# Optimization experiments

Hardware: AMD Instinct MI355X
Metric: run time of the kernel (lower is better)

The kernel has to match this reference:

```python
import jax, jax.numpy as jnp
import numpy as np

B, H, S, D = 1, 16, 2048, 64
KQ_PRE, KK_PRE = 6, 11      # pre-softmax conv kernel (query x key)
KQ_POST, KK_POST = 3, 3     # post-softmax conv kernel


def depthwise_causal_conv(x, w):
    """Per-head 2D conv over score tensor x:[B,H,Q,K], w:[H,kq,kk].
    Causal padding: only past queries (pad top kq-1) and past keys (pad left kk-1)."""
    h, kq, kk = w.shape
    return jax.lax.conv_general_dilated(
        x, w[:, None, :, :],  # [H,1,kq,kk] depthwise
        window_strides=(1, 1),
        padding=[(kq - 1, 0), (kk - 1, 0)],
        dimension_numbers=("NCHW", "OIHW", "NCHW"),
        feature_group_count=h,
    )


def setup_inputs() -> dict:
    key = jax.random.key(0)
    ks = jax.random.split(key, 8)
    eye = jnp.eye(H, dtype=jnp.float32)
    return {
        "xq": jax.random.normal(ks[0], (B, H, S, D), jnp.float32),
        "xk": jax.random.normal(ks[1], (B, H, S, D), jnp.float32),
        "xv": jax.random.normal(ks[2], (B, H, S, D), jnp.float32),
        "mask": jnp.zeros((1,), jnp.float32),  # unused (use_mask=False)
        "w_conv_pre": 0.1 * jax.random.normal(ks[3], (H, KQ_PRE, KK_PRE), jnp.float32),
        "w_conv_post": 0.1 * jax.random.normal(ks[4], (H, KQ_POST, KK_POST), jnp.float32),
        "w_psm": eye + 0.02 * jax.random.normal(ks[5], (H, H), jnp.float32),
        "w_posm": eye + 0.02 * jax.random.normal(ks[6], (H, H), jnp.float32),
    }


def reference(xq, xk, xv, mask, w_conv_pre, w_conv_post, w_psm, w_posm):
    del mask  # use_mask=False path
    b, h, q, d = xq.shape
    k = xk.shape[2]
    causal = jnp.arange(k)[None, :] <= jnp.arange(q)[:, None]  # [Q,K] True = visible
    scale = 1.0 / jnp.sqrt(jnp.float32(d))

    # QK^T scores
    scores = jnp.einsum("bhqd,bhkd->bhqk", xq, xk) * scale
    # pre-softmax causal depthwise conv (future entries zeroed going in)
    scores = depthwise_causal_conv(jnp.where(causal, scores, 0.0), w_conv_pre)
    # pre-softmax per-head linear mixing; masked region -> -inf (output_value)
    scores = jnp.einsum("gh,bhqk->bgqk", w_psm, scores)
    scores = jnp.where(causal, scores, -jnp.inf)

    probs = jax.nn.softmax(scores.astype(jnp.float32), axis=-1).astype(xq.dtype)

    # post-softmax causal depthwise conv
    probs = depthwise_causal_conv(jnp.where(causal, probs, 0.0), w_conv_post)
    probs = jnp.where(causal, probs, 0.0)
    # post-softmax per-head linear mixing; masked region -> 0
    probs = jnp.einsum("gh,bhqk->bgqk", w_posm, probs)
    probs = jnp.where(causal, probs, 0.0)

    # attention output, transposed to [B,S,H,D]
    out = jnp.einsum("bhqk,bhkd->bqhd", probs, xv)
    return out
```

## Files before the change

### kernel.cpp

```cpp
#include <hip/hip_runtime.h>
#include <math.h>

#define H 16
#define S 2048
#define D 64
#define SCALEQK 0.125f
#define CH 256

typedef __attribute__((ext_vector_type(4))) float f32x4;
typedef __attribute__((ext_vector_type(8))) short bf16x8;
typedef __attribute__((ext_vector_type(8))) _Float16 f16x8;
typedef __attribute__((ext_vector_type(4))) _Float16 f16x4;
typedef __attribute__((ext_vector_type(2))) _Float16 f16x2;

__device__ inline float h2f(unsigned short b) {
    _Float16 h; __builtin_memcpy(&h, &b, 2); return (float)h;
}
__device__ inline unsigned short f2h(float x) {
    _Float16 h = (_Float16)x; unsigned short b; __builtin_memcpy(&b, &h, 2); return b;
}
__device__ inline unsigned int pack2h(float a, float b) {
    return (unsigned int)f2h(a) | ((unsigned int)f2h(b) << 16);
}

__device__ inline float fdot2f(unsigned int a, unsigned int b, float c) {
#if __has_builtin(__builtin_amdgcn_fdot2)
    f16x2 av, bv;
    __builtin_memcpy(&av, &a, 4);
    __builtin_memcpy(&bv, &b, 4);
    return __builtin_amdgcn_fdot2(av, bv, c, false);
#else
    return c + h2f((unsigned short)(a & 0xffff)) * h2f((unsigned short)(b & 0xffff))
             + h2f((unsigned short)(a >> 16))    * h2f((unsigned short)(b >> 16));
#endif
}

__device__ inline void stage_hilo(float4 a, float4 b, uint4* vh, uint4* vl) {
    float xs[8] = {a.x, a.y, a.z, a.w, b.x, b.y, b.z, b.w};
    unsigned int hh[8], ll[8];
#pragma unroll
    for (int j = 0; j < 8; ++j) {
        unsigned int u = __float_as_uint(xs[j]);
        unsigned int h = (u + 0x7fffu + ((u >> 16) & 1u)) >> 16;
        float r = xs[j] - __uint_as_float(h << 16);
        unsigned int u2 = __float_as_uint(r);
        hh[j] = h;
        ll[j] = (u2 + 0x7fffu + ((u2 >> 16) & 1u)) >> 16;
    }
    uint4 h4, l4;
    h4.x = hh[0] | (hh[1] << 16); h4.y = hh[2] | (hh[3] << 16);
    h4.z = hh[4] | (hh[5] << 16); h4.w = hh[6] | (hh[7] << 16);
    l4.x = ll[0] | (ll[1] << 16); l4.y = ll[2] | (ll[3] << 16);
    l4.z = ll[4] | (ll[5] << 16); l4.w = ll[6] | (ll[7] << 16);
    *vh = h4; *vl = l4;
}

__device__ inline void online_upd(float& m, float& l, float x) {
    if (x > m) { l = l * __expf(m - x) + 1.f; m = x; }
    else       { l += __expf(x - m); }
}

__global__ __launch_bounds__(256) void mta_cvt_kernel(const float* __restrict__ src,
                                                      unsigned short* __restrict__ hi,
                                                      unsigned short* __restrict__ lo,
                                                      float scale, int n8) {
    int i = blockIdx.x * 256 + threadIdx.x;
    int stride = gridDim.x * 256;
    for (; i < n8; i += stride) {
        const float* p = src + (size_t)i * 8;
        float4 a = *(const float4*)p;
        float4 b = *(const float4*)(p + 4);
        a.x *= scale; a.y *= scale; a.z *= scale; a.w *= scale;
        b.x *= scale; b.y *= scale; b.z *= scale; b.w *= scale;
        uint4 vh, vl; stage_hilo(a, b, &vh, &vl);
        *(uint4*)&hi[(size_t)i * 8] = vh;
        *(uint4*)&lo[(size_t)i * 8] = vl;
    }
}

__global__ __launch_bounds__(256) void mta_vt_kernel(const float* __restrict__ xv,
                                                     unsigned short* __restrict__ vt) {
    const int kt = blockIdx.x, f = blockIdx.y;
    const int tid = threadIdx.x;
    __shared__ unsigned short lt[64][65];
#pragma unroll
    for (int i = 0; i < 16; ++i) {
        int idx = tid + i * 256;
        int r = idx >> 6, c = idx & 63;
        lt[r][c] = f2h(xv[((size_t)f * S + kt * 64 + r) * D + c]);
    }
    __syncthreads();
#pragma unroll
    for (int i = 0; i < 16; ++i) {
        int idx = tid + i * 256;
        int d = idx >> 6, k = idx & 63;
        vt[((size_t)f * D + d) * S + kt * 64 + k] = lt[k][d];
    }
}

__global__ __launch_bounds__(256) void mta_gemm_kernel(
        const unsigned short* __restrict__ qhi, const unsigned short* __restrict__ qlo,
        const unsigned short* __restrict__ khi, const unsigned short* __restrict__ klo,
        unsigned short* __restrict__ R, int qs, int SQ) {
    const int kt = blockIdx.x, qt = blockIdx.y, h = blockIdx.z;
    const int q0 = qs - 64 + qt * 64;
    const int k0 = kt * 64;
    if (k0 > q0 + 68) return;
    const int tid = threadIdx.x;
    const int SQ64 = SQ + 64;

    __shared__ unsigned short Qs[2][64][72];
    __shared__ unsigned short Ks[2][64][72];
    __shared__ unsigned short Ro[64][72];

    {
        int r = tid >> 2, d = (tid & 3) * 16;
        int gq = q0 + r;
        uint4 z = {0u, 0u, 0u, 0u};
        uint4 a0 = z, a1 = z, b0 = z, b1 = z;
        if (gq >= 0) {
            size_t off = ((size_t)h * S + gq) * D + d;
            a0 = *(const uint4*)&qhi[off]; a1 = *(const uint4*)&qhi[off + 8];
            b0 = *(const uint4*)&qlo[off]; b1 = *(const uint4*)&qlo[off + 8];
        }
        *(uint4*)&Qs[0][r][d] = a0; *(uint4*)&Qs[0][r][d + 8] = a1;
        *(uint4*)&Qs[1][r][d] = b0; *(uint4*)&Qs[1][r][d + 8] = b1;
        size_t offk = ((size_t)h * S + (k0 + r)) * D + d;
        uint4 c0 = *(const uint4*)&khi[offk];
        uint4 c1 = *(const uint4*)&khi[offk + 8];
        uint4 d0 = *(const uint4*)&klo[offk];
        uint4 d1 = *(const uint4*)&klo[offk + 8];
        *(uint4*)&Ks[0][r][d] = c0; *(uint4*)&Ks[0][r][d + 8] = c1;
        *(uint4*)&Ks[1][r][d] = d0; *(uint4*)&Ks[1][r][d + 8] = d1;
    }
    __syncthreads();

    const int w = tid >> 6, lane = tid & 63;
    const int wr = w >> 1, wc = w & 1;
    const int lr = lane & 15, lk = lane >> 4;

    f32x4 acc[2][2];
#pragma unroll
    for (int mi = 0; mi < 2; ++mi)
#pragma unroll
        for (int ni = 0; ni < 2; ++ni) acc[mi][ni] = (f32x4){0.f, 0.f, 0.f, 0.f};

#pragma unroll
    for (int ks = 0; ks < 2; ++ks) {
        int db = ks * 32 + lk * 8;
#pragma unroll
        for (int mi = 0; mi < 2; ++mi) {
            bf16x8 ah = *(const bf16x8*)&Qs[0][wr * 32 + mi * 16 + lr][db];
            bf16x8 al = *(const bf16x8*)&Qs[1][wr * 32 + mi * 16 + lr][db];
#pragma unroll
            for (int ni = 0; ni < 2; ++ni) {
                bf16x8 bh = *(const bf16x8*)&Ks[0][wc * 32 + ni * 16 + lr][db];
                bf16x8 bl = *(const bf16x8*)&Ks[1][wc * 32 + ni * 16 + lr][db];
                acc[mi][ni] = __builtin_amdgcn_mfma_f32_16x16x32_bf16(ah, bh, acc[mi][ni], 0, 0, 0);
                acc[mi][ni] = __builtin_amdgcn_mfma_f32_16x16x32_bf16(ah, bl, acc[mi][ni], 0, 0, 0);
                acc[mi][ni] = __builtin_amdgcn_mfma_f32_16x16x32_bf16(al, bh, acc[mi][ni], 0, 0, 0);
            }
        }
    }

#pragma unroll
    for (int mi = 0; mi < 2; ++mi)
#pragma unroll
        for (int ni = 0; ni < 2; ++ni)
#pragma unroll
            for (int i = 0; i < 4; ++i) {
                int row = wr * 32 + mi * 16 + lk * 4 + i;
                int col = wc * 32 + ni * 16 + lr;
                int gq = q0 + row, gk = k0 + col;
                Ro[row][col] = f2h((gk <= gq) ? acc[mi][ni][i] : 0.f);
            }
    __syncthreads();

#pragma unroll
    for (int ii = 0; ii < 2; ++ii) {
        int idx = tid + ii * 256;
        int row = idx >> 3, c8 = (idx & 7) * 8;
        int lrow = qt * 64 + row;
        *(uint4*)&R[((size_t)h * SQ64 + lrow) * S + k0 + c8] = *(const uint4*)&Ro[row][c8];
    }
}

__global__ __launch_bounds__(256) void mta_convmix_kernel(
        const unsigned short* __restrict__ R,
        const float* __restrict__ w_pre, const float* __restrict__ w_psm,
        unsigned short* __restrict__ sc, int qs, int SQ) {
    const int kc = blockIdx.x, qt = blockIdx.y;
    const int q0 = qs - 16 + qt * 16;
    const int k0 = kc * 64;
    if (k0 > q0 + 15) return;
    const int tid = threadIdx.x;
    const int SQ64 = SQ + 64;

    __shared__ unsigned short raw_u16[2][2][21][88];
    __shared__ unsigned short co[1024][16];
    __shared__ unsigned int wpk[16][6][6];
    __shared__ unsigned short wpsmf[16][16];

    for (int idx = tid; idx < 576; idx += 256) {
        int h = idx / 36, i2 = (idx % 36) / 6, ip = idx % 6;
        float w0 = w_pre[h * 66 + i2 * 11 + ip * 2];
        float w1 = (ip < 5) ? w_pre[h * 66 + i2 * 11 + ip * 2 + 1] : 0.f;
        wpk[h][i2][ip] = pack2h(w0, w1);
    }
    wpsmf[tid >> 4][tid & 15] = f2h(w_psm[tid]);

    const int ql = tid & 15;
    const int kb = (tid >> 4) * 4;

    const int sr = tid / 10, sc8 = tid % 10;
    const bool sact = (tid < 210);
    const bool sval = sact && (k0 + sc8 * 8 >= 16);
    const size_t srow_off = (size_t)(qt * 16 + sr + 43) * S + (k0 - 16 + sc8 * 8);

    uint4 sA = {0u, 0u, 0u, 0u}, sB = {0u, 0u, 0u, 0u};

#define LOADC(hh, dst) do { \
        if (sval) dst = *(const uint4*)&R[(size_t)(hh) * SQ64 * S + srow_off]; \
        else { dst.x = 0u; dst.y = 0u; dst.z = 0u; dst.w = 0u; } \
    } while (0)

#define WRITEC(bb, tt, src) do { if (sact) { \
        *(uint4*)&raw_u16[bb][tt][sr][sc8 * 8] = src; } \
    } while (0)

#define CONVC(hh, bb, tt) do { \
        float c0_ = 0.f, c1_ = 0.f, c2_ = 0.f, c3_ = 0.f; \
        _Pragma("unroll") \
        for (int i2_ = 0; i2_ < 6; ++i2_) { \
            const unsigned int* rp_ = \
                (const unsigned int*)&raw_u16[bb][tt][ql + i2_][0] + (kb / 2 + 3); \
            unsigned int P_[7]; \
            _Pragma("unroll") \
            for (int i_ = 0; i_ < 7; ++i_) P_[i_] = rp_[i_]; \
            unsigned int Sv_[6]; \
            _Pragma("unroll") \
            for (int i_ = 0; i_ < 6; ++i_) Sv_[i_] = (P_[i_] >> 16) | (P_[i_ + 1] << 16); \
            unsigned int T_ = P_[6] >> 16; \
            const unsigned int* wp_ = &wpk[hh][i2_][0]; \
            _Pragma("unroll") \
            for (int i_ = 0; i_ < 6; ++i_) { \
                unsigned int w_ = wp_[i_]; \
                c0_ = fdot2f(w_, P_[i_], c0_); \
                c1_ = fdot2f(w_, Sv_[i_], c1_); \
                c2_ = fdot2f(w_, P_[i_ + 1], c2_); \
                c3_ = fdot2f(w_, (i_ < 5) ? Sv_[i_ + 1] : T_, c3_); \
            } \
        } \
        { float cc_[4] = {c0_, c1_, c2_, c3_}; \
          int p0_ = ql * 64 + kb; \
          _Pragma("unroll") \
          for (int j_ = 0; j_ < 4; ++j_) { \
              int pp_ = p0_ + j_; \
              int x_ = ((pp_ >> 2) ^ (pp_ >> 6)) & 3; \
              co[pp_][(hh) ^ (x_ << 2)] = f2h(cc_[j_]); } } \
    } while (0)

    LOADC(0, sA);
    LOADC(1, sB);
    WRITEC(0, 0, sA);
    WRITEC(0, 1, sB);
    __syncthreads();
    for (int ph = 0; ph < 8; ++ph) {
        int bb = ph & 1;
        if (ph < 7) { LOADC(2 * ph + 2, sA); LOADC(2 * ph + 3, sB); }
        CONVC(2 * ph,     bb, 0);
        CONVC(2 * ph + 1, bb, 1);
        if (ph < 7) { WRITEC(bb ^ 1, 0, sA); WRITEC(bb ^ 1, 1, sB); }
        __syncthreads();
    }
#undef LOADC
#undef WRITEC
#undef CONVC

    const int lane = tid & 63, wv = tid >> 6;
    const int hg = lane >> 4;
#if __has_builtin(__builtin_amdgcn_mfma_f32_16x16x16f16)
    f16x4 afrag = *(const f16x4*)&wpsmf[lane & 15][hg * 4];
    for (int t = wv; t < 64; t += 4) {
        int p = t * 16 + (lane & 15);
        int x = ((p >> 2) ^ (p >> 6)) & 3;
        f16x4 bfrag = *(const f16x4*)&co[p][(hg ^ x) << 2];
        f32x4 d = {0.f, 0.f, 0.f, 0.f};
        d = __builtin_amdgcn_mfma_f32_16x16x16f16(afrag, bfrag, d, 0, 0, 0);
        int qq = q0 + (p >> 6);
        int kk = k0 + (p & 63);
        int srow = qt * 16 + (p >> 6);
#pragma unroll
        for (int i = 0; i < 4; ++i) {
            int g = hg * 4 + i;
            sc[((size_t)(g * (SQ + 16) + srow)) * S + kk] =
                f2h((kk <= qq) ? d[i] : 0.f);
        }
    }
#else
    for (int t = wv; t < 64; t += 4) {
        int p = t * 16 + (lane & 15);
        int x = ((p >> 2) ^ (p >> 6)) & 3;
        float ch[16];
#pragma unroll
        for (int a = 0; a < 4; ++a) {
            f16x4 b4 = *(const f16x4*)&co[p][(a ^ x) << 2];
#pragma unroll
            for (int tt = 0; tt < 4; ++tt) ch[a * 4 + tt] = (float)b4[tt];
        }
        int qq = q0 + (p >> 6);
        int kk = k0 + (p & 63);
        int srow = qt * 16 + (p >> 6);
#pragma unroll
        for (int i = 0; i < 4; ++i) {
            int g = hg * 4 + i;
            float s = 0.f;
#pragma unroll
            for (int hh = 0; hh < 16; ++hh) s += h2f(wpsmf[g][hh]) * ch[hh];
            sc[((size_t)(g * (SQ + 16) + srow)) * S + kk] =
                f2h((kk <= qq) ? s : 0.f);
        }
    }
#endif
}

__global__ __launch_bounds__(256) void mta_rowstats_kernel(
        const unsigned short* __restrict__ sc,
        float* __restrict__ mrow, float* __restrict__ rlrow, int qs, int SQ) {
    int row = blockIdx.x * 4 + (threadIdx.x >> 6);
    int lane = threadIdx.x & 63;
    int g = row / SQ, qq = row % SQ;
    int q = qs + qq;
    const unsigned short* rp = sc + ((size_t)(g * (SQ + 16) + qq + 16)) * S;

    float v[32];
#pragma unroll
    for (int it = 0; it < 4; ++it) {
        int kbase = it * 512 + lane * 8;
        if (it * 512 <= q) {
            uint4 u = *(const uint4*)&rp[kbase];
            unsigned int ws[4] = {u.x, u.y, u.z, u.w};
#pragma unroll
            for (int j = 0; j < 4; ++j) {
                float x0 = h2f((unsigned short)(ws[j] & 0xffff));
                float x1 = h2f((unsigned short)(ws[j] >> 16));
                v[it * 8 + 2 * j]     = (kbase + 2 * j     <= q) ? x0 : -INFINITY;
                v[it * 8 + 2 * j + 1] = (kbase + 2 * j + 1 <= q) ? x1 : -INFINITY;
            }
        } else {
#pragma unroll
            for (int j = 0; j < 8; ++j) v[it * 8 + j] = -INFINITY;
        }
    }
    float m = -INFINITY;
#pragma unroll
    for (int j = 0; j < 32; ++j) m = fmaxf(m, v[j]);
#pragma unroll
    for (int off = 1; off < 64; off <<= 1) m = fmaxf(m, __shfl_xor(m, off));
    float l = 0.f;
#pragma unroll
    for (int j = 0; j < 32; ++j) l += __expf(v[j] - m);
#pragma unroll
    for (int off = 1; off < 64; off <<= 1) l += __shfl_xor(l, off);
    if (lane == 0) { mrow[g * S + q] = m; rlrow[g * S + q] = 1.f / l; }
}

__global__ __launch_bounds__(256) void mta_out2_kernel(
        const unsigned short* __restrict__ sc,
        const float* __restrict__ mrow, const float* __restrict__ rlrow,
        const unsigned short* __restrict__ vt,
        const float* __restrict__ w_post, const float* __restrict__ w_posm,
        float* __restrict__ out, int qs, int SQ) {
    const int qt = blockIdx.x, kc = blockIdx.y;
    const int q0 = qs + qt * 16;
    const int kstart = kc * CH;
    if (kstart > q0 + 15) return;
    const int kend = min(kstart + CH, q0 + 16);
    const int tid = threadIdx.x;

    __shared__ unsigned short ps[16][18][36];
    __shared__ unsigned short pm2[16][16][40];
    __shared__ float mst[16][18], rst[16][18];
    __shared__ float wpost_s[144], wposm_s[256];

    wposm_s[tid] = w_posm[tid];
    if (tid < 144) wpost_s[tid] = w_post[tid];
    for (int i = tid; i < 288; i += 256) {
        int g = i / 18, r = i % 18;
        int qp = q0 - 2 + r;
        if (qp >= 0) { mst[g][r] = mrow[g * S + qp]; rst[g][r] = rlrow[g * S + qp]; }
        else         { mst[g][r] = 0.f; rst[g][r] = 0.f; }
    }

    const int ql = tid >> 4, kb = (tid & 15) * 2;
    const int wv = tid >> 6, lane = tid & 63;
    const int lr = lane & 15, lk = lane >> 4;

    f32x4 acc[4][4];
#pragma unroll
    for (int a = 0; a < 4; ++a)
#pragma unroll
        for (int b = 0; b < 4; ++b) acc[a][b] = (f32x4){0.f, 0.f, 0.f, 0.f};

    __syncthreads();

    for (int k0 = kstart; k0 < kend; k0 += 32) {
        for (int i = tid; i < 4896; i += 256) {
            int g = i / 306, rem = i % 306;
            int r = rem / 17, c2 = (rem % 17) * 2;
            int qp = q0 - 2 + r;
            int kp = k0 - 2 + c2;
            float p0 = 0.f, p1 = 0.f;
            if (qp >= 0 && kp >= 0) {
                unsigned int u = *(const unsigned int*)
                    &sc[((size_t)(g * (SQ + 16) + qp - (qs - 16))) * S + kp];
                float mm = mst[g][r], rr = rst[g][r];
                if (kp <= qp)     p0 = __expf(h2f((unsigned short)(u & 0xffff)) - mm) * rr;
                if (kp + 1 <= qp) p1 = __expf(h2f((unsigned short)(u >> 16)) - mm) * rr;
            }
            *(unsigned int*)&ps[g][r][c2] = pack2h(p0, p1);
        }
        __syncthreads();

        {
            float cg0[16], cg1[16];
#pragma unroll
            for (int g = 0; g < 16; ++g) {
                float c0 = 0.f, c1 = 0.f;
#pragma unroll
                for (int i2 = 0; i2 < 3; ++i2) {
                    unsigned int u0 = *(const unsigned int*)&ps[g][ql + i2][kb];
                    unsigned int u1 = *(const unsigned int*)&ps[g][ql + i2][kb + 2];
                    float v0 = h2f((unsigned short)(u0 & 0xffff));
                    float v1 = h2f((unsigned short)(u0 >> 16));
                    float v2 = h2f((unsigned short)(u1 & 0xffff));
                    float v3 = h2f((unsigned short)(u1 >> 16));
                    const float* wp = &wpost_s[g * 9 + i2 * 3];
                    c0 += wp[0] * v0 + wp[1] * v1 + wp[2] * v2;
                    c1 += wp[0] * v1 + wp[1] * v2 + wp[2] * v3;
                }
                cg0[g] = c0; cg1[g] = c1;
            }
            int q = q0 + ql, k = k0 + kb;
            bool val0 = (k <= q) && (k < kend);
            bool val1 = (k + 1 <= q) && (k + 1 < kend);
#pragma unroll
            for (int ff = 0; ff < 16; ++ff) {
                float s0 = 0.f, s1 = 0.f;
#pragma unroll
                for (int g = 0; g < 16; ++g) {
                    float w = wposm_s[ff * 16 + g];
                    s0 += w * cg0[g]; s1 += w * cg1[g];
                }
                *(unsigned int*)&pm2[ff][ql][kb] = pack2h(val0 ? s0 : 0.f, val1 ? s1 : 0.f);
            }
        }
        __syncthreads();

#pragma unroll
        for (int hh = 0; hh < 4; ++hh) {
            int f = wv * 4 + hh;
            f16x8 a = *(const f16x8*)&pm2[f][lr][lk * 8];
#pragma unroll
            for (int tc = 0; tc < 4; ++tc) {
                uint4 braw = *(const uint4*)
                    &vt[((size_t)(f * D + tc * 16 + lr)) * S + k0 + lk * 8];
                f16x8 b;
                __builtin_memcpy(&b, &braw, 16);
                acc[hh][tc] = __builtin_amdgcn_mfma_f32_16x16x32_f16(a, b, acc[hh][tc], 0, 0, 0);
            }
        }
    }

#pragma unroll
    for (int hh = 0; hh < 4; ++hh) {
        int f = wv * 4 + hh;
#pragma unroll
        for (int tc = 0; tc < 4; ++tc) {
#pragma unroll
            for (int i = 0; i < 4; ++i) {
                int q = q0 + lk * 4 + i;
                int d = tc * 16 + lr;
                atomicAdd(&out[((size_t)q * H + f) * D + d], acc[hh][tc][i]);
            }
        }
    }
}

__global__ __launch_bounds__(256) void fb_stats_kernel(
        const float* __restrict__ xq, const float* __restrict__ xk,
        const float* __restrict__ w_pre, const float* __restrict__ w_psm,
        float* __restrict__ mpart, float* __restrict__ lpart) {
    const int kc = blockIdx.x, qt = blockIdx.y;
    const int q0 = qt * 16;
    const int kstart = kc * CH;
    if (kstart > q0 + 15) return;
    const int kend = min(kstart + CH, q0 + 16);
    const int tid = threadIdx.x;

    __shared__ unsigned short Qs[2][32][72];
    __shared__ unsigned short Ks[2][48][72];
    __shared__ float raws[32][50];
    __shared__ float wpre_s[16 * 66];
    __shared__ float wpsm_s[256];

    for (int i = tid; i < 16 * 66; i += 256) wpre_s[i] = w_pre[i];
    wpsm_s[tid] = w_psm[tid];

    const int ql = tid >> 4;
    const int kb = (tid & 15) * 2;
    const int q = q0 + ql;

    float mreg[16], lreg[16];
#pragma unroll
    for (int g = 0; g < 16; ++g) { mreg[g] = -INFINITY; lreg[g] = 0.f; }

    for (int k0 = kstart; k0 < kend; k0 += 32) {
        float acc0[16], acc1[16];
#pragma unroll
        for (int g = 0; g < 16; ++g) { acc0[g] = 0.f; acc1[g] = 0.f; }

        for (int h = 0; h < H; ++h) {
            {
                int r = tid >> 3, d = (tid & 7) * 8;
                int qp = q0 - 5 + r;
                float4 a = {0,0,0,0}, b = {0,0,0,0};
                if (r < 21 && qp >= 0) {
                    const float* p = &xq[(h * S + qp) * D + d];
                    a = *(const float4*)p; b = *(const float4*)(p + 4);
                }
                uint4 vh, vl; stage_hilo(a, b, &vh, &vl);
                *(uint4*)&Qs[0][r][d] = vh;
                *(uint4*)&Qs[1][r][d] = vl;
            }
            for (int i = tid; i < 384; i += 256) {
                int r = i >> 3, d = (i & 7) * 8;
                int kp = k0 - 10 + r;
                float4 a = {0,0,0,0}, b = {0,0,0,0};
                if (r < 42 && kp >= 0) {
                    const float* p = &xk[(h * S + kp) * D + d];
                    a = *(const float4*)p; b = *(const float4*)(p + 4);
                }
                uint4 vh, vl; stage_hilo(a, b, &vh, &vl);
                *(uint4*)&Ks[0][r][d] = vh;
                *(uint4*)&Ks[1][r][d] = vl;
            }
            __syncthreads();
            {
                int w = tid >> 6, l = tid & 63;
                int lr = l & 15, lk = l >> 4;
                for (int t = w; t < 6; t += 4) {
                    int tr = t / 3, tc = t % 3;
                    f32x4 acc = {0.f, 0.f, 0.f, 0.f};
#pragma unroll
                    for (int ks = 0; ks < 2; ++ks) {
                        int db = ks * 32 + lk * 8;
                        bf16x8 ah = *(const bf16x8*)&Qs[0][tr * 16 + lr][db];
                        bf16x8 al = *(const bf16x8*)&Qs[1][tr * 16 + lr][db];
                        bf16x8 bh = *(const bf16x8*)&Ks[0][tc * 16 + lr][db];
                        bf16x8 bl = *(const bf16x8*)&Ks[1][tc * 16 + lr][db];
                        acc = __builtin_amdgcn_mfma_f32_16x16x32_bf16(ah, bh, acc, 0, 0, 0);
                        acc = __builtin_amdgcn_mfma_f32_16x16x32_bf16(ah, bl, acc, 0, 0, 0);
                        acc = __builtin_amdgcn_mfma_f32_16x16x32_bf16(al, bh, acc, 0, 0, 0);
                    }
#pragma unroll
                    for (int i = 0; i < 4; ++i) {
                        int row = tr * 16 + lk * 4 + i;
                        int col = tc * 16 + lr;
                        int qp = q0 - 5 + row, kp = k0 - 10 + col;
                        raws[row][col] = (kp >= 0 && kp <= qp) ? acc[i] * SCALEQK : 0.f;
                    }
                }
            }
            __syncthreads();
            {
                float c0 = 0.f, c1 = 0.f;
#pragma unroll
                for (int i2 = 0; i2 < 6; ++i2) {
                    const float* rp = &raws[ql + i2][kb];
                    float v[12];
#pragma unroll
                    for (int j = 0; j < 6; ++j) {
                        float2 t = *(const float2*)(rp + 2 * j);
                        v[2 * j] = t.x; v[2 * j + 1] = t.y;
                    }
                    const float* wp = &wpre_s[h * 66 + i2 * 11];
#pragma unroll
                    for (int j = 0; j < 11; ++j) { c0 += wp[j] * v[j]; c1 += wp[j] * v[j + 1]; }
                }
#pragma unroll
                for (int g = 0; g < 16; ++g) {
                    float wg = wpsm_s[g * 16 + h];
                    acc0[g] += wg * c0; acc1[g] += wg * c1;
                }
            }
        }
        int kk = k0 + kb;
#pragma unroll
        for (int g = 0; g < 16; ++g) {
            if (kk <= q)     online_upd(mreg[g], lreg[g], acc0[g]);
            if (kk + 1 <= q) online_upd(mreg[g], lreg[g], acc1[g]);
        }
    }
#pragma unroll
    for (int g = 0; g < 16; ++g) {
        float m = mreg[g], l = lreg[g];
#pragma unroll
        for (int off = 1; off < 16; off <<= 1) {
            float m2 = __shfl_xor(m, off);
            float l2 = __shfl_xor(l, off);
            float nm = fmaxf(m, m2);
            float t1 = (l  > 0.f) ? l  * __expf(m  - nm) : 0.f;
            float t2 = (l2 > 0.f) ? l2 * __expf(m2 - nm) : 0.f;
            m = nm; l = t1 + t2;
        }
        if ((tid & 15) == 0) {
            mpart[((size_t)kc * H + g) * S + q] = m;
            lpart[((size_t)kc * H + g) * S + q] = l;
        }
    }
}

__global__ __launch_bounds__(256) void fb_reduce_kernel(
        const float* __restrict__ mpart, const float* __restrict__ lpart,
        float* __restrict__ mrow, float* __restrict__ rlrow) {
    int r = blockIdx.x * 256 + threadIdx.x;
    if (r >= H * S) return;
    int q = r & (S - 1);
    int nkc = (q >> 8) + 1;
    float m = -INFINITY;
    for (int kc = 0; kc < nkc; ++kc) m = fmaxf(m, mpart[(size_t)kc * H * S + r]);
    float l = 0.f;
    for (int kc = 0; kc < nkc; ++kc) {
        float li = lpart[(size_t)kc * H * S + r];
        float mi = mpart[(size_t)kc * H * S + r];
        if (li > 0.f) l += li * __expf(mi - m);
    }
    mrow[r] = m;
    rlrow[r] = 1.f / l;
}

__global__ __launch_bounds__(256) void fb_out_kernel(
        const float* __restrict__ xq, const float* __restrict__ xk,
        const float* __restrict__ xv,
        const float* __restrict__ w_pre, const float* __restrict__ w_psm,
        const float* __restrict__ w_post, const float* __restrict__ w_posm,
        const float* __restrict__ mrow, const float* __restrict__ rlrow,
        float* __restrict__ out) {
    const int qt = blockIdx.x, kc = blockIdx.y;
    const int q0 = qt * 8;
    const int kstart = kc * CH;
    if (kstart > q0 + 7) return;
    const int kend = min(kstart + CH, q0 + 8);
    const int tid = threadIdx.x;

    __shared__ unsigned short Qs[2][16][72];
    __shared__ unsigned short Ks[2][48][72];
    __shared__ float raws[16][50];
    __shared__ float ps[8][10][35];
    __shared__ float m2s[16][8][33];
    __shared__ float mst[16][10], rst[16][10];
    __shared__ float wpre_s[16 * 66], wpsm_s[256], wpost_s[144], wposm_s[256];

    for (int i = tid; i < 16 * 66; i += 256) wpre_s[i] = w_pre[i];
    wpsm_s[tid] = w_psm[tid];
    wposm_s[tid] = w_posm[tid];
    if (tid < 144) wpost_s[tid] = w_post[tid];
    for (int i = tid; i < 160; i += 256) {
        int g = i / 10, r = i % 10;
        int qp = q0 - 2 + r;
        if (qp >= 0) { mst[g][r] = mrow[g * S + qp]; rst[g][r] = rlrow[g * S + qp]; }
        else         { mst[g][r] = 0.f; rst[g][r] = 0.f; }
    }

    const int f = tid >> 4, qloc = (tid >> 1) & 7, dh = tid & 1;
    const int cr = tid / 17, cc = (tid % 17) * 2;
    const bool cvalid = tid < 170;
    const int ql2 = tid >> 5, kl = tid & 31;

    float oacc[32];
#pragma unroll
    for (int i = 0; i < 32; ++i) oacc[i] = 0.f;

    for (int k0 = kstart; k0 < kend; k0 += 32) {
        float a0[16], a1[16];
#pragma unroll
        for (int g = 0; g < 16; ++g) { a0[g] = 0.f; a1[g] = 0.f; }

        for (int h = 0; h < H; ++h) {
            if (tid < 128) {
                int r = tid >> 3, d = (tid & 7) * 8;
                int qp = q0 - 7 + r;
                float4 a = {0,0,0,0}, b = {0,0,0,0};
                if (qp >= 0 && qp < S) {
                    const float* p = &xq[(h * S + qp) * D + d];
                    a = *(const float4*)p; b = *(const float4*)(p + 4);
                }
                uint4 vh, vl; stage_hilo(a, b, &vh, &vl);
                *(uint4*)&Qs[0][r][d] = vh;
                *(uint4*)&Qs[1][r][d] = vl;
            }
            for (int i = tid; i < 384; i += 256) {
                int r = i >> 3, d = (i & 7) * 8;
                int kp = k0 - 12 + r;
                float4 a = {0,0,0,0}, b = {0,0,0,0};
                if (kp >= 0 && kp < S) {
                    const float* p = &xk[(h * S + kp) * D + d];
                    a = *(const float4*)p; b = *(const float4*)(p + 4);
                }
                uint4 vh, vl; stage_hilo(a, b, &vh, &vl);
                *(uint4*)&Ks[0][r][d] = vh;
                *(uint4*)&Ks[1][r][d] = vl;
            }
            __syncthreads();
            {
                int w = tid >> 6, l = tid & 63;
                int lr = l & 15, lk = l >> 4;
                if (w < 3) {
                    int tc = w;
                    f32x4 acc = {0.f, 0.f, 0.f, 0.f};
#pragma unroll
                    for (int ks = 0; ks < 2; ++ks) {
                        int db = ks * 32 + lk * 8;
                        bf16x8 ah = *(const bf16x8*)&Qs[0][lr][db];
                        bf16x8 al = *(const bf16x8*)&Qs[1][lr][db];
                        bf16x8 bh = *(const bf16x8*)&Ks[0][tc * 16 + lr][db];
                        bf16x8 bl = *(const bf16x8*)&Ks[1][tc * 16 + lr][db];
                        acc = __builtin_amdgcn_mfma_f32_16x16x32_bf16(ah, bh, acc, 0, 0, 0);
                        acc = __builtin_amdgcn_mfma_f32_16x16x32_bf16(ah, bl, acc, 0, 0, 0);
                        acc = __builtin_amdgcn_mfma_f32_16x16x32_bf16(al, bh, acc, 0, 0, 0);
                    }
#pragma unroll
                    for (int i = 0; i < 4; ++i) {
                        int row = lk * 4 + i, col = tc * 16 + lr;
                        int qp = q0 - 7 + row, kp = k0 - 12 + col;
                        raws[row][col] = (kp >= 0 && kp <= qp) ? acc[i] * SCALEQK : 0.f;
                    }
                }
            }
            __syncthreads();
            if (cvalid) {
                float c0 = 0.f, c1 = 0.f;
#pragma unroll
                for (int i2 = 0; i2 < 6; ++i2) {
                    const float* rp = &raws[cr + i2][cc];
                    float v[12];
#pragma unroll
                    for (int j = 0; j < 6; ++j) {
                        float2 t = *(const float2*)(rp + 2 * j);
                        v[2 * j] = t.x; v[2 * j + 1] = t.y;
                    }
                    const float* wp = &wpre_s[h * 66 + i2 * 11];
#pragma unroll
                    for (int j = 0; j < 11; ++j) { c0 += wp[j] * v[j]; c1 += wp[j] * v[j + 1]; }
                }
#pragma unroll
                for (int g = 0; g < 16; ++g) {
                    float wg = wpsm_s[g * 16 + h];
                    a0[g] += wg * c0; a1[g] += wg * c1;
                }
            }
        }

        float m2f[16];
#pragma unroll
        for (int i = 0; i < 16; ++i) m2f[i] = 0.f;

        for (int half = 0; half < 2; ++half) {
            if (cvalid) {
                int qp = q0 - 2 + cr;
                int kp0 = k0 - 2 + cc, kp1 = kp0 + 1;
#pragma unroll
                for (int g8 = 0; g8 < 8; ++g8) {
                    int g = half * 8 + g8;
                    float p0 = 0.f, p1 = 0.f;
                    if (qp >= 0) {
                        float mm = mst[g][cr], rr = rst[g][cr];
                        if (kp0 >= 0 && kp0 <= qp) p0 = __expf(a0[g] - mm) * rr;
                        if (kp1 >= 0 && kp1 <= qp) p1 = __expf(a1[g] - mm) * rr;
                    }
                    ps[g8][cr][cc] = p0;
                    ps[g8][cr][cc + 1] = p1;
                }
            }
            __syncthreads();
            {
                float cg[8];
#pragma unroll
                for (int g8 = 0; g8 < 8; ++g8) {
                    float c = 0.f;
#pragma unroll
                    for (int i2 = 0; i2 < 3; ++i2)
#pragma unroll
                        for (int j2 = 0; j2 < 3; ++j2)
                            c += wpost_s[(half * 8 + g8) * 9 + i2 * 3 + j2] * ps[g8][ql2 + i2][kl + j2];
                    cg[g8] = c;
                }
#pragma unroll
                for (int ff = 0; ff < 16; ++ff) {
                    float s = 0.f;
#pragma unroll
                    for (int g8 = 0; g8 < 8; ++g8) s += wposm_s[ff * 16 + half * 8 + g8] * cg[g8];
                    m2f[ff] += s;
                }
            }
            if (half == 0) __syncthreads();
        }
        {
            int q = q0 + ql2, k = k0 + kl;
            bool valid = (k <= q) && (k < kend);
#pragma unroll
            for (int ff = 0; ff < 16; ++ff) m2s[ff][ql2][kl] = valid ? m2f[ff] : 0.f;
        }
        __syncthreads();
        for (int kl2 = 0; kl2 < 32; ++kl2) {
            int k = k0 + kl2;
            if (k >= kend) break;
            float s = m2s[f][qloc][kl2];
            if (s != 0.f) {
                const float* vp = &xv[(f * S + k) * D + dh * 32];
#pragma unroll
                for (int d4 = 0; d4 < 8; ++d4) {
                    float4 v = *(const float4*)(vp + d4 * 4);
                    oacc[d4 * 4 + 0] += s * v.x;
                    oacc[d4 * 4 + 1] += s * v.y;
                    oacc[d4 * 4 + 2] += s * v.z;
                    oacc[d4 * 4 + 3] += s * v.w;
                }
            }
        }
        __syncthreads();
    }

    int q = q0 + qloc;
    float* op = out + ((size_t)q * H + f) * D + dh * 32;
#pragma unroll
    for (int i = 0; i < 32; ++i) atomicAdd(op + i, oacc[i]);
}

extern "C" void kernel_launch(void* const* d_in, const int* in_sizes, int n_in,
                              void* d_out, int out_size, void* d_ws, size_t ws_size,
                              hipStream_t stream) {
    const float* xq     = (const float*)d_in[0];
    const float* xk     = (const float*)d_in[1];
    const float* xv     = (const float*)d_in[2];
    const float* w_pre  = (const float*)d_in[4];
    const float* w_post = (const float*)d_in[5];
    const float* w_psm  = (const float*)d_in[6];
    const float* w_posm = (const float*)d_in[7];
    float* out = (float*)d_out;

    hipMemsetAsync(d_out, 0, sizeof(float) * (size_t)out_size, stream);

    const size_t qkb   = (size_t)H * S * D * 2;
    const size_t vtb   = (size_t)H * D * S * 2;
    const size_t statb = (size_t)H * S * 4;
    const size_t base  = 4 * qkb + vtb + 2 * statb;

    int SQ = 0;
    const int cands[5] = {2048, 1024, 512, 256, 128};
    for (int c = 0; c < 5; ++c) {
        size_t rb  = (size_t)H * (cands[c] + 64) * S * 2;
        size_t scb = (size_t)H * (cands[c] + 16) * S * 2;
        if (base + rb + scb <= ws_size) { SQ = cands[c]; break; }
    }

    if (SQ == 0) {
        float* mpart = (float*)d_ws;
        float* lpart = mpart + (size_t)8 * H * S;
        float* mrow  = lpart + (size_t)8 * H * S;
        float* rlrow = mrow + (size_t)H * S;
        dim3 g1(8, 128);
        fb_stats_kernel<<<g1, 256, 0, stream>>>(xq, xk, w_pre, w_psm, mpart, lpart);
        fb_reduce_kernel<<<128, 256, 0, stream>>>(mpart, lpart, mrow, rlrow);
        dim3 g2(256, 8);
        fb_out_kernel<<<g2, 256, 0, stream>>>(xq, xk, xv, w_pre, w_psm, w_post, w_posm,
                                              mrow, rlrow, out);
        return;
    }

    char* p = (char*)d_ws;
    unsigned short* qhi = (unsigned short*)p;            p += qkb;
    unsigned short* qlo = (unsigned short*)p;            p += qkb;
    unsigned short* khi = (unsigned short*)p;            p += qkb;
    unsigned short* klo = (unsigned short*)p;            p += qkb;
    unsigned short* vt  = (unsigned short*)p;            p += vtb;
    float* mrow  = (float*)p;                            p += statb;
    float* rlrow = (float*)p;                            p += statb;
    unsigned short* Rbuf = (unsigned short*)p;           p += (size_t)H * (SQ + 64) * S * 2;
    unsigned short* sc   = (unsigned short*)p;

    const int n8 = H * S * D / 8;
    mta_cvt_kernel<<<512, 256, 0, stream>>>(xq, qhi, qlo, SCALEQK, n8);
    mta_cvt_kernel<<<512, 256, 0, stream>>>(xk, khi, klo, 1.0f, n8);
    dim3 gv(S / 64, H);
    mta_vt_kernel<<<gv, 256, 0, stream>>>(xv, vt);

    for (int qs = 0; qs < S; qs += SQ) {
        dim3 gg(S / 64, SQ / 64 + 1, H);
        mta_gemm_kernel<<<gg, 256, 0, stream>>>(qhi, qlo, khi, klo, Rbuf, qs, SQ);
        dim3 gc(S / 64, SQ / 16 + 1);
        mta_convmix_kernel<<<gc, 256, 0, stream>>>(Rbuf, w_pre, w_psm, sc, qs, SQ);
        mta_rowstats_kernel<<<4 * SQ, 256, 0, stream>>>(sc, mrow, rlrow, qs, SQ);
        dim3 g2(SQ / 16, 8);
        mta_out2_kernel<<<g2, 256, 0, stream>>>(sc, mrow, rlrow, vt, w_post, w_posm,
                                                out, qs, SQ);
    }
}
```

Baseline: 497.5 us.

## Use MFMA for post-softmax head mixing and alias score/mix LDS buffers

Replaces the scalar 16x16 per-head mixing of post-softmax conv outputs with a 16x16x16 f16 MFMA. Conv results are staged in a swizzled LDS buffer, and the mixing weights are held in registers as an A fragment. The ps and pm2 shared buffers now alias one array to cut LDS footprint, which adds an extra barrier per k-chunk. Mixing inputs and weights are rounded to fp16 before accumulation, a small precision change.

```diff
diff --git a/kernel.cpp b/kernel.cpp
--- a/kernel.cpp
+++ b/kernel.cpp
@@ -378,12 +378,16 @@
     const int kend = min(kstart + CH, q0 + 16);
     const int tid = threadIdx.x;
 
-    __shared__ unsigned short ps[16][18][36];
-    __shared__ unsigned short pm2[16][16][40];
+    __shared__ unsigned short uni[10368];
+    __shared__ unsigned short co[512][16];
     __shared__ float mst[16][18], rst[16][18];
-    __shared__ float wpost_s[144], wposm_s[256];
-
-    wposm_s[tid] = w_posm[tid];
+    __shared__ float wpost_s[144];
+    __shared__ unsigned short wposmf[16][16];
+
+#define PS(g, r, c)  uni[((g) * 18 + (r)) * 36 + (c)]
+#define PM2(f, r, c) uni[((f) * 16 + (r)) * 40 + (c)]
+
+    wposmf[tid >> 4][tid & 15] = f2h(w_posm[tid]);
     if (tid < 144) wpost_s[tid] = w_post[tid];
     for (int i = tid; i < 288; i += 256) {
         int g = i / 18, r = i % 18;
@@ -395,6 +399,7 @@
     const int ql = tid >> 4, kb = (tid & 15) * 2;
     const int wv = tid >> 6, lane = tid & 63;
     const int lr = lane & 15, lk = lane >> 4;
+    const int hg = lk;
 
     f32x4 acc[4][4];
 #pragma unroll
@@ -403,6 +408,10 @@
         for (int b = 0; b < 4; ++b) acc[a][b] = (f32x4){0.f, 0.f, 0.f, 0.f};
 
     __syncthreads();
+
+#if __has_builtin(__builtin_amdgcn_mfma_f32_16x16x16f16)
+    f16x4 afrag = *(const f16x4*)&wposmf[lane & 15][hg * 4];
+#endif
 
     for (int k0 = kstart; k0 < kend; k0 += 32) {
         for (int i = tid; i < 4896; i += 256) {
@@ -418,7 +427,7 @@
                 if (kp <= qp)     p0 = __expf(h2f((unsigned short)(u & 0xffff)) - mm) * rr;
                 if (kp + 1 <= qp) p1 = __expf(h2f((unsigned short)(u >> 16)) - mm) * rr;
             }
-            *(unsigned int*)&ps[g][r][c2] = pack2h(p0, p1);
+            *(unsigned int*)&PS(g, r, c2) = pack2h(p0, p1);
         }
         __syncthreads();
 
@@ -429,8 +438,8 @@
                 float c0 = 0.f, c1 = 0.f;
 #pragma unroll
                 for (int i2 = 0; i2 < 3; ++i2) {
-                    unsigned int u0 = *(const unsigned int*)&ps[g][ql + i2][kb];
-                    unsigned int u1 = *(const unsigned int*)&ps[g][ql + i2][kb + 2];
+                    unsigned int u0 = *(const unsigned int*)&PS(g, ql + i2, kb);
+                    unsigned int u1 = *(const unsigned int*)&PS(g, ql + i2, kb + 2);
                     float v0 = h2f((unsigned short)(u0 & 0xffff));
                     float v1 = h2f((unsigned short)(u0 >> 16));
                     float v2 = h2f((unsigned short)(u1 & 0xffff));
@@ -441,26 +450,64 @@
                 }
                 cg0[g] = c0; cg1[g] = c1;
             }
-            int q = q0 + ql, k = k0 + kb;
-            bool val0 = (k <= q) && (k < kend);
-            bool val1 = (k + 1 <= q) && (k + 1 < kend);
-#pragma unroll
-            for (int ff = 0; ff < 16; ++ff) {
-                float s0 = 0.f, s1 = 0.f;
-#pragma unroll
-                for (int g = 0; g < 16; ++g) {
-                    float w = wposm_s[ff * 16 + g];
-                    s0 += w * cg0[g]; s1 += w * cg1[g];
-                }
-                *(unsigned int*)&pm2[ff][ql][kb] = pack2h(val0 ? s0 : 0.f, val1 ? s1 : 0.f);
-            }
-        }
+            int p0 = ql * 32 + kb;
+#pragma unroll
+            for (int j = 0; j < 2; ++j) {
+                int pp = p0 + j;
+                int x = ((pp >> 2) ^ (pp >> 5)) & 3;
+#pragma unroll
+                for (int g = 0; g < 16; ++g)
+                    co[pp][g ^ (x << 2)] = f2h(j ? cg1[g] : cg0[g]);
+            }
+        }
+        __syncthreads();
+
+#if __has_builtin(__builtin_amdgcn_mfma_f32_16x16x16f16)
+        for (int t = wv; t < 32; t += 4) {
+            int p = t * 16 + (lane & 15);
+            int x = ((p >> 2) ^ (p >> 5)) & 3;
+            f16x4 bfrag = *(const f16x4*)&co[p][(hg ^ x) << 2];
+            f32x4 d = {0.f, 0.f, 0.f, 0.f};
+            d = __builtin_amdgcn_mfma_f32_16x16x16f16(afrag, bfrag, d, 0, 0, 0);
+            int prow = p >> 5, pcol = p & 31;
+            int q = q0 + prow, k = k0 + pcol;
+            bool valid = (k <= q) && (k < kend);
+#pragma unroll
+            for (int i = 0; i < 4; ++i) {
+                int f = hg * 4 + i;
+                PM2(f, prow, pcol) = f2h(valid ? d[i] : 0.f);
+            }
+        }
+#else
+        for (int t = wv; t < 32; t += 4) {
+            int p = t * 16 + (lane & 15);
+            int x = ((p >> 2) ^ (p >> 5)) & 3;
+            float ch[16];
+#pragma unroll
+            for (int a = 0; a < 4; ++a) {
+                f16x4 b4 = *(const f16x4*)&co[p][(a ^ x) << 2];
+#pragma unroll
+                for (int tt = 0; tt < 4; ++tt) ch[a * 4 + tt] = (float)b4[tt];
+            }
+            int prow = p >> 5, pcol = p & 31;
+            int q = q0 + prow, k = k0 + pcol;
+            bool valid = (k <= q) && (k < kend);
+#pragma unroll
+            for (int i = 0; i < 4; ++i) {
+                int f = hg * 4 + i;
+                float s = 0.f;
+#pragma unroll
+                for (int g = 0; g < 16; ++g) s += h2f(wposmf[f][g]) * ch[g];
+                PM2(f, prow, pcol) = f2h(valid ? s : 0.f);
+            }
+        }
+#endif
         __syncthreads();
 
 #pragma unroll
         for (int hh = 0; hh < 4; ++hh) {
             int f = wv * 4 + hh;
-            f16x8 a = *(const f16x8*)&pm2[f][lr][lk * 8];
+            f16x8 a = *(const f16x8*)&PM2(f, lr, lk * 8);
 #pragma unroll
             for (int tc = 0; tc < 4; ++tc) {
                 uint4 braw = *(const uint4*)
@@ -470,6 +517,7 @@
                 acc[hh][tc] = __builtin_amdgcn_mfma_f32_16x16x32_f16(a, b, acc[hh][tc], 0, 0, 0);
             }
         }
+        __syncthreads();
     }
 
 #pragma unroll
@@ -485,6 +533,8 @@
             }
         }
     }
+#undef PS
+#undef PM2
 }
 
 __global__ __launch_bounds__(256) void fb_stats_kernel(
```

After: 571.3 us. 1.15x slower.
